# Performance work log

Measured on AMD Instinct MI355X. Metric: run time of the kernel, lower is better.

Reference implementation:

```python
import jax, jax.numpy as jnp
import jax.scipy as jsp
import numpy as np

H, W, C = 2048, 2048, 3
SCALE, TRANSLATE, ROTATE, SHEAR = 1.15, 0.15, np.pi / 12, 0.0


def _rotation_matrix(r):
    rx, ry = jnp.cos(r), jnp.sin(r)
    return jnp.array([[rx, ry, 0.0], [-ry, rx, 0.0], [0.0, 0.0, 1.0]])


def _scale_matrix(s):
    return jnp.array([[s, 0.0, 0.0], [0.0, s, 0.0], [0.0, 0.0, 1.0]])


def _shear_matrix(r):
    sh = jnp.tan(r)
    return jnp.array([[1.0, sh, 0.0], [0.0, 1.0, 0.0], [0.0, 0.0, 1.0]])


def _translation_matrix(tx, ty):
    return jnp.array([[1.0, 0.0, tx], [0.0, 1.0, ty], [0.0, 0.0, 1.0]])


def setup_inputs() -> dict:
    key = jax.random.key(0)
    k_img, k1, k2, k3, k4, k5 = jax.random.split(key, 6)
    image = jax.random.normal(k_img, (H, W, C), dtype=jnp.float32)
    # Random affine params exactly as RandomAffine.__call__ samples them.
    scale = jax.random.uniform(k1, minval=1.0, maxval=SCALE)
    tx = jax.random.uniform(k2, minval=-TRANSLATE, maxval=TRANSLATE) * W
    ty = jax.random.uniform(k3, minval=-TRANSLATE, maxval=TRANSLATE) * H
    rotation = jax.random.uniform(k4, minval=-1.0, maxval=1.0) * ROTATE
    shear = jax.random.uniform(k5, minval=-1.0, maxval=1.0) * SHEAR
    matrix = (_rotation_matrix(rotation) @ _scale_matrix(scale)
              @ _shear_matrix(shear) @ _translation_matrix(tx, ty))
    return {"image": image, "matrix": matrix.astype(jnp.float32)}


def _apply_affine(image, matrix):
    h, w, c = image.shape
    dtype = image.dtype
    y = jnp.linspace(-h / 2, h / 2, num=h)
    x = jnp.linspace(-w / 2, w / 2, num=w)
    v = jnp.ones(1)
    ch = jnp.arange(3)
    # (h, w, 1, 3, 4) grid of homogeneous coords [y, x, 1, channel]
    coords = jnp.stack(jnp.meshgrid(y, x, v, ch, indexing='ij'), axis=-1).astype(dtype)
    transform = jnp.eye(4, dtype=dtype).at[:-1, :-1].set(matrix.astype(dtype))
    coords = coords @ transform + jnp.array([h / 2, w / 2, 0.0, 0.0], dtype=dtype)
    # drop the homogeneous slot (index -2), keep (y, x, channel)
    coords = jnp.concatenate([coords[..., :2], coords[..., 3:]], axis=-1)
    # 'h w v c yxc -> yxc (h w v c)'
    coords = coords.reshape(-1, 3).T  # (3, h*w*3)
    out = jsp.ndimage.map_coordinates(
        image, [coords[0], coords[1], coords[2]], order=1, mode='reflect')
    return out.reshape(h, w, c)


def reference(image, matrix):
    return _apply_affine(image, matrix)
```

## Files before the change

### kernel.cpp

```cpp
#include <hip/hip_runtime.h>


#define IMG_H 2048
#define IMG_W 2048
#define TILE  32
#define NT    8
#define BBH   48
#define NV4   39
#define BBW3  (NV4 * 4)
#define BUFN  (BBH * BBW3)

__device__ __forceinline__ int reflect2048(int i) {
    int p = i & 4095;
    return (p < 2048) ? p : (4095 - p);
}

__device__ __forceinline__ void gl2lds16(const float* g, float* l) {
    __builtin_amdgcn_global_load_lds(
        (const __attribute__((address_space(1))) void*)g,
        (__attribute__((address_space(3))) void*)l,
        16, 0, 0);
}

__global__ __launch_bounds__(256) void affine_dbuf_kernel(
    const float* __restrict__ img, const float* __restrict__ Mp,
    float* __restrict__ out)
{
    __shared__ float lds[2][BUFN];

    const int tid = threadIdx.x;
    const int grp = blockIdx.x & 7;
    const int tby = blockIdx.x >> 3;
    const int i0 = tby * TILE;
    const int j0base = grp * (TILE * NT);

    const float step = 2048.0f / 2047.0f;
    const float m00 = Mp[0], m01 = Mp[1];
    const float m10 = Mp[3], m11 = Mp[4];
    const float b0 = Mp[6] + 1024.0f, b1 = Mp[7] + 1024.0f;

    const float yv0 = fmaf((float)i0,            step, -1024.0f);
    const float yv1 = fmaf((float)(i0 + TILE-1), step, -1024.0f);

    auto bbox = [&](int j0, int& y0, int& x0, int& nrows, int& nv4, bool& fast) {
        const float xva = fmaf((float)j0,          step, -1024.0f);
        const float xvb = fmaf((float)(j0+TILE-1), step, -1024.0f);
        const float rya = yv0*m00 + xva*m10 + b0, ryb = yv0*m00 + xvb*m10 + b0;
        const float ryc = yv1*m00 + xva*m10 + b0, ryd = yv1*m00 + xvb*m10 + b0;
        const float rxa = yv0*m01 + xva*m11 + b1, rxb = yv0*m01 + xvb*m11 + b1;
        const float rxc = yv1*m01 + xva*m11 + b1, rxd = yv1*m01 + xvb*m11 + b1;
        const float miny = fminf(fminf(rya,ryb), fminf(ryc,ryd));
        const float maxy = fmaxf(fmaxf(rya,ryb), fmaxf(ryc,ryd));
        const float minx = fminf(fminf(rxa,rxb), fminf(rxc,rxd));
        const float maxx = fmaxf(fmaxf(rxa,rxb), fmaxf(rxc,rxd));
        y0 = (int)floorf(miny) - 1;
        nrows = (int)floorf(maxy) + 3 - y0;
        x0 = ((int)floorf(minx) - 1) & ~3;
        const int xw = (int)floorf(maxx) + 3 - x0;
        nv4 = (xw * 3 + 3) >> 2;
        fast = (x0 >= 0) && (x0*3 + nv4*4 <= IMG_W*3);
    };

    auto dmafill = [&](float* buf, int y0, int x0, int nrows, int nv4) {
        const int wid = tid >> 6, lane = tid & 63;
        if (lane < nv4) {
            for (int r = wid; r < nrows; r += 4) {
                const int gy = reflect2048(y0 + r);
                gl2lds16(img + gy*(IMG_W*3) + x0*3 + lane*4, &buf[r*BBW3]);
            }
        }
    };
    auto slowfill = [&](float* buf, int y0, int x0, int nrows) {
        for (int e = tid; e < nrows*52; e += 256) {
            const int r  = e / 52;
            const int xx = e - r*52;
            const int gy = reflect2048(y0 + r);
            const int gx = reflect2048(x0 + xx);
            const float* s = img + (gy*IMG_W + gx)*3;
            float* d = &buf[r*BBW3 + xx*3];
            d[0] = s[0]; d[1] = s[1]; d[2] = s[2];
        }
    };

    auto compute = [&](const float* buf, int j0, int y0, int x0) {
        const int row = tid >> 3;
        const int col = (tid & 7) * 4;
        const int i = i0 + row;
        const float yv = fmaf((float)i, step, -1024.0f);
        float v[12];
        #pragma unroll
        for (int k = 0; k < 4; ++k) {
            const float xv = fmaf((float)(j0 + col + k), step, -1024.0f);
            const float ry = yv*m00 + xv*m10 + b0;
            const float rx = yv*m01 + xv*m11 + b1;
            const float fy = floorf(ry), fx = floorf(rx);
            const float wy1 = ry - fy, wx1 = rx - fx;
            const float wy0 = 1.0f - wy1, wx0 = 1.0f - wx1;
            const int iy = (int)fy - y0;
            const int ix = (int)fx - x0;
            const float* p0 = &buf[iy*BBW3 + ix*3];
            const float* p1 = p0 + BBW3;
            const float w00 = wy0*wx0, w01 = wy0*wx1;
            const float w10 = wy1*wx0, w11 = wy1*wx1;
            v[k*3+0] = w00*p0[0] + w01*p0[3] + w10*p1[0] + w11*p1[3];
            v[k*3+1] = w00*p0[1] + w01*p0[4] + w10*p1[1] + w11*p1[4];
            v[k*3+2] = w00*p0[2] + w01*p0[5] + w10*p1[2] + w11*p1[5];
        }
        float* ob = out + (i*IMG_W + j0 + col)*3;
        *(float4*)(ob+0) = make_float4(v[0], v[1], v[2],  v[3]);
        *(float4*)(ob+4) = make_float4(v[4], v[5], v[6],  v[7]);
        *(float4*)(ob+8) = make_float4(v[8], v[9], v[10], v[11]);
    };

    int y0c, x0c, nrc, nvc; bool fc;
    bbox(j0base, y0c, x0c, nrc, nvc, fc);
    if (fc) dmafill(lds[0], y0c, x0c, nrc, nvc);
    else    slowfill(lds[0], y0c, x0c, nrc);
    __syncthreads();

    int cur = 0;
    for (int t = 0; t < NT; ++t) {
        const int j0 = j0base + t*TILE;
        int y0n, x0n, nrn, nvn; bool fn = false;
        if (t+1 < NT) {
            bbox(j0 + TILE, y0n, x0n, nrn, nvn, fn);
            if (fn) dmafill(lds[cur^1], y0n, x0n, nrn, nvn);
            else    slowfill(lds[cur^1], y0n, x0n, nrn);
        }
        compute(lds[cur], j0, y0c, x0c);
        __syncthreads();
        y0c = y0n; x0c = x0n; cur ^= 1;
    }
}

extern "C" void kernel_launch(void* const* d_in, const int* in_sizes, int n_in,
                              void* d_out, int out_size, void* d_ws, size_t ws_size,
                              hipStream_t stream) {
    const float* img = (const float*)d_in[0];
    const float* M   = (const float*)d_in[1];
    float* out = (float*)d_out;

    dim3 grid((IMG_H / TILE) * (IMG_W / (TILE * NT))), block(256);
    hipLaunchKernelGGL(affine_dbuf_kernel, grid, block, 0, stream, img, M, out);
}
```

Before: 121.9 us.

## Shrink tile to 16x32 and compute one pixel per thread per pass

Cuts the output tile height from 32 to 16 rows, which shrinks the LDS staging buffer (32 rows x 37 float4) and doubles the number of blocks. The compute loop changes from four adjacent pixels per thread with float4 stores to two passes of one pixel per thread with scalar stores. Row and column counts are clamped to the buffer size. The smaller LDS footprint should raise occupancy and cut redundant bounding-box halo loads per block. In exchange the output stores become uncoalesced scalar writes, and the clamps can drop needed source pixels if the bounding box exceeds the buffer.

New measurement: 113.7 us. 1.07x faster.

```diff
diff --git a/kernel.cpp b/kernel.cpp
--- a/kernel.cpp
+++ b/kernel.cpp
@@ -3,12 +3,13 @@
 
 #define IMG_H 2048
 #define IMG_W 2048
-#define TILE  32
+#define TH    16
+#define TW    32
 #define NT    8
-#define BBH   48
-#define NV4   39
-#define BBW3  (NV4 * 4)
-#define BUFN  (BBH * BBW3)
+#define BBH   32
+#define NV4C  37
+#define STR   (NV4C * 4)
+#define BUFN  (BBH * STR)
 
 __device__ __forceinline__ int reflect2048(int i) {
     int p = i & 4095;
@@ -22,7 +23,7 @@
         16, 0, 0);
 }
 
-__global__ __launch_bounds__(256) void affine_dbuf_kernel(
+__global__ __launch_bounds__(256) void affine_dbuf16_kernel(
     const float* __restrict__ img, const float* __restrict__ Mp,
     float* __restrict__ out)
 {
@@ -31,20 +32,20 @@
     const int tid = threadIdx.x;
     const int grp = blockIdx.x & 7;
     const int tby = blockIdx.x >> 3;
-    const int i0 = tby * TILE;
-    const int j0base = grp * (TILE * NT);
+    const int i0 = tby * TH;
+    const int j0base = grp * (TW * NT);
 
     const float step = 2048.0f / 2047.0f;
     const float m00 = Mp[0], m01 = Mp[1];
     const float m10 = Mp[3], m11 = Mp[4];
     const float b0 = Mp[6] + 1024.0f, b1 = Mp[7] + 1024.0f;
 
-    const float yv0 = fmaf((float)i0,            step, -1024.0f);
-    const float yv1 = fmaf((float)(i0 + TILE-1), step, -1024.0f);
+    const float yv0 = fmaf((float)i0,          step, -1024.0f);
+    const float yv1 = fmaf((float)(i0 + TH-1), step, -1024.0f);
 
     auto bbox = [&](int j0, int& y0, int& x0, int& nrows, int& nv4, bool& fast) {
-        const float xva = fmaf((float)j0,          step, -1024.0f);
-        const float xvb = fmaf((float)(j0+TILE-1), step, -1024.0f);
+        const float xva = fmaf((float)j0,        step, -1024.0f);
+        const float xvb = fmaf((float)(j0+TW-1), step, -1024.0f);
         const float rya = yv0*m00 + xva*m10 + b0, ryb = yv0*m00 + xvb*m10 + b0;
         const float ryc = yv1*m00 + xva*m10 + b0, ryd = yv1*m00 + xvb*m10 + b0;
         const float rxa = yv0*m01 + xva*m11 + b1, rxb = yv0*m01 + xvb*m11 + b1;
@@ -55,9 +56,11 @@
         const float maxx = fmaxf(fmaxf(rxa,rxb), fmaxf(rxc,rxd));
         y0 = (int)floorf(miny) - 1;
         nrows = (int)floorf(maxy) + 3 - y0;
+        if (nrows > BBH) nrows = BBH;
         x0 = ((int)floorf(minx) - 1) & ~3;
         const int xw = (int)floorf(maxx) + 3 - x0;
         nv4 = (xw * 3 + 3) >> 2;
+        if (nv4 > NV4C) nv4 = NV4C;
         fast = (x0 >= 0) && (x0*3 + nv4*4 <= IMG_W*3);
     };
 
@@ -66,31 +69,30 @@
         if (lane < nv4) {
             for (int r = wid; r < nrows; r += 4) {
                 const int gy = reflect2048(y0 + r);
-                gl2lds16(img + gy*(IMG_W*3) + x0*3 + lane*4, &buf[r*BBW3]);
+                gl2lds16(img + gy*(IMG_W*3) + x0*3 + lane*4, &buf[r*STR]);
             }
         }
     };
     auto slowfill = [&](float* buf, int y0, int x0, int nrows) {
-        for (int e = tid; e < nrows*52; e += 256) {
-            const int r  = e / 52;
-            const int xx = e - r*52;
+        for (int e = tid; e < nrows*48; e += 256) {
+            const int r  = e / 48;
+            const int xx = e - r*48;
             const int gy = reflect2048(y0 + r);
             const int gx = reflect2048(x0 + xx);
             const float* s = img + (gy*IMG_W + gx)*3;
-            float* d = &buf[r*BBW3 + xx*3];
+            float* d = &buf[r*STR + xx*3];
             d[0] = s[0]; d[1] = s[1]; d[2] = s[2];
         }
     };
 
     auto compute = [&](const float* buf, int j0, int y0, int x0) {
-        const int row = tid >> 3;
-        const int col = (tid & 7) * 4;
-        const int i = i0 + row;
-        const float yv = fmaf((float)i, step, -1024.0f);
-        float v[12];
         #pragma unroll
-        for (int k = 0; k < 4; ++k) {
-            const float xv = fmaf((float)(j0 + col + k), step, -1024.0f);
+        for (int pass = 0; pass < 2; ++pass) {
+            const int row = pass*8 + (tid >> 5);
+            const int col = tid & 31;
+            const int i = i0 + row, j = j0 + col;
+            const float yv = fmaf((float)i, step, -1024.0f);
+            const float xv = fmaf((float)j, step, -1024.0f);
             const float ry = yv*m00 + xv*m10 + b0;
             const float rx = yv*m01 + xv*m11 + b1;
             const float fy = floorf(ry), fx = floorf(rx);
@@ -98,18 +100,15 @@
             const float wy0 = 1.0f - wy1, wx0 = 1.0f - wx1;
             const int iy = (int)fy - y0;
             const int ix = (int)fx - x0;
-            const float* p0 = &buf[iy*BBW3 + ix*3];
-            const float* p1 = p0 + BBW3;
+            const float* p0 = &buf[iy*STR + ix*3];
+            const float* p1 = p0 + STR;
             const float w00 = wy0*wx0, w01 = wy0*wx1;
             const float w10 = wy1*wx0, w11 = wy1*wx1;
-            v[k*3+0] = w00*p0[0] + w01*p0[3] + w10*p1[0] + w11*p1[3];
-            v[k*3+1] = w00*p0[1] + w01*p0[4] + w10*p1[1] + w11*p1[4];
-            v[k*3+2] = w00*p0[2] + w01*p0[5] + w10*p1[2] + w11*p1[5];
+            float* ob = out + (i*IMG_W + j)*3;
+            ob[0] = w00*p0[0] + w01*p0[3] + w10*p1[0] + w11*p1[3];
+            ob[1] = w00*p0[1] + w01*p0[4] + w10*p1[1] + w11*p1[4];
+            ob[2] = w00*p0[2] + w01*p0[5] + w10*p1[2] + w11*p1[5];
         }
-        float* ob = out + (i*IMG_W + j0 + col)*3;
-        *(float4*)(ob+0) = make_float4(v[0], v[1], v[2],  v[3]);
-        *(float4*)(ob+4) = make_float4(v[4], v[5], v[6],  v[7]);
-        *(float4*)(ob+8) = make_float4(v[8], v[9], v[10], v[11]);
     };
 
     int y0c, x0c, nrc, nvc; bool fc;
@@ -120,10 +119,10 @@
 
     int cur = 0;
     for (int t = 0; t < NT; ++t) {
-        const int j0 = j0base + t*TILE;
+        const int j0 = j0base + t*TW;
         int y0n, x0n, nrn, nvn; bool fn = false;
         if (t+1 < NT) {
-            bbox(j0 + TILE, y0n, x0n, nrn, nvn, fn);
+            bbox(j0 + TW, y0n, x0n, nrn, nvn, fn);
             if (fn) dmafill(lds[cur^1], y0n, x0n, nrn, nvn);
             else    slowfill(lds[cur^1], y0n, x0n, nrn);
         }
@@ -140,6 +139,6 @@
     const float* M   = (const float*)d_in[1];
     float* out = (float*)d_out;
 
-    dim3 grid((IMG_H / TILE) * (IMG_W / (TILE * NT))), block(256);
-    hipLaunchKernelGGL(affine_dbuf_kernel, grid, block, 0, stream, img, M, out);
+    dim3 grid((IMG_H / TH) * (IMG_W / (TW * NT))), block(256);
+    hipLaunchKernelGGL(affine_dbuf16_kernel, grid, block, 0, stream, img, M, out);
 }
```
